# Performance work log

Hardware: AMD Instinct MI355X
Metric: run time of the kernel (lower is better)

## Reference

```python
import jax, jax.numpy as jnp
import numpy as np

B, S, I, E, D = 64, 512, 64, 256, 256  # batch, src_len, input_size, enc_hid, dec_hid


def _lstm_cell(h, c, x, Wih, Whh, b):
    # PyTorch LSTM gate order: i, f, g, o ; b = b_ih + b_hh combined
    z = x @ Wih.T + h @ Whh.T + b
    i, f, g, o = jnp.split(z, 4, axis=-1)
    c = jax.nn.sigmoid(f) * c + jax.nn.sigmoid(i) * jnp.tanh(g)
    h = jax.nn.sigmoid(o) * jnp.tanh(c)
    return h, c


def _run_lstm(x, h0, c0, Wih, Whh, b):
    # x: [B,S,I] -> outputs [B,S,H]
    def step(carry, xt):
        h, c = _lstm_cell(carry[0], carry[1], xt, Wih, Whh, b)
        return (h, c), h
    _, ys = jax.lax.scan(step, (h0, c0), jnp.swapaxes(x, 0, 1))
    return jnp.swapaxes(ys, 0, 1)


def _forward(x, enc_h0, enc_c0, dec_h0, dec_c0, Wih_f, Whh_f, b_f, Wih_b, Whh_b, b_b,
             W_attn, b_attn, v, Wih_d, Whh_d, b_d, W_lin, b_lin):
    b_, s_ = x.shape[0], x.shape[1]
    # bidirectional encoder
    out_f = _run_lstm(x, enc_h0[0], enc_c0[0], Wih_f, Whh_f, b_f)
    out_b = _run_lstm(x[:, ::-1, :], enc_h0[1], enc_c0[1], Wih_b, Whh_b, b_b)[:, ::-1, :]
    enc_out = jnp.concatenate([out_f, out_b], axis=-1)  # [B,S,2E]
    h0d, c0d = dec_h0[0], dec_c0[0]  # decoder re-starts from these EVERY step (faithful)

    @jax.checkpoint
    def dec_step(carry, _):
        y, h_attn = carry  # y: [B,1], h_attn: [B,D]
        dh = h_attn.shape[-1]
        cat = jnp.concatenate(
            [jnp.broadcast_to(h_attn[:, None, :], (b_, s_, dh)), enc_out], axis=-1)
        energy = jnp.tanh(cat @ W_attn.T + b_attn)              # [B,S,D]
        attn = jax.nn.softmax(jnp.einsum('d,bsd->bs', v, energy), axis=1)
        context = jnp.einsum('bs,bse->be', attn, enc_out)       # [B,2E]
        dec_in = jnp.concatenate([y, context], axis=-1)         # [B,1+2E]
        h_new, _c = _lstm_cell(h0d, c0d, dec_in, Wih_d, Whh_d, b_d)
        y_new = jnp.concatenate([h_new, context], axis=-1) @ W_lin.T + b_lin  # [B,1]
        return (y_new, h_new), y_new

    y0 = jnp.zeros((b_, 1), dtype=x.dtype)
    _, ys = jax.lax.scan(dec_step, (y0, h0d), None, length=s_)  # [S,B,1]
    # output_size == 1, so torch's cat-then-[:,1:] equals the stacked per-step ys
    return jnp.swapaxes(ys, 0, 1).reshape(b_, s_)


def setup_inputs() -> dict:
    key = jax.random.key(0)
    ks = jax.random.split(key, 20)
    W = 0.05  # weight scale ~ torch default init magnitude
    rn = lambda k, sh, s: jax.random.normal(k, sh, dtype=jnp.float32) * s
    return {
        'x': rn(ks[0], (B, S, I), 1.0),
        'enc_h0': rn(ks[1], (2, B, E), 1.0),
        'enc_c0': rn(ks[2], (2, B, E), 1.0),
        'dec_h0': rn(ks[3], (1, B, D), 1.0),
        'dec_c0': rn(ks[4], (1, B, D), 1.0),
        'Wih_f': rn(ks[5], (4 * E, I), W),
        'Whh_f': rn(ks[6], (4 * E, E), W),
        'b_f': rn(ks[7], (4 * E,), W),
        'Wih_b': rn(ks[8], (4 * E, I), W),
        'Whh_b': rn(ks[9], (4 * E, E), W),
        'b_b': rn(ks[10], (4 * E,), W),
        'W_attn': rn(ks[11], (D, D + 2 * E), W),
        'b_attn': rn(ks[12], (D,), W),
        'v': jax.random.uniform(ks[13], (D,), dtype=jnp.float32),
        'Wih_d': rn(ks[14], (4 * D, 2 * E + 1), W),
        'Whh_d': rn(ks[15], (4 * D, D), W),
        'b_d': rn(ks[16], (4 * D,), W),
        'W_lin': rn(ks[17], (1, 2 * E + D), W),
        'b_lin': rn(ks[18], (1,), W),
    }


def reference(x, enc_h0, enc_c0, dec_h0, dec_c0, Wih_f, Whh_f, b_f, Wih_b, Whh_b, b_b,
              W_attn, b_attn, v, Wih_d, Whh_d, b_d, W_lin, b_lin):
    return _forward(x, enc_h0, enc_c0, dec_h0, dec_c0, Wih_f, Whh_f, b_f,
                    Wih_b, Whh_b, b_b, W_attn, b_attn, v, Wih_d, Whh_d, b_d,
                    W_lin, b_lin)
```

## Files before the change

### kernel.cpp

```cpp
#include <hip/hip_runtime.h>
#include <hip/hip_bf16.h>

#define NB 64
#define NS 512
#define NI 64
#define NE 256
#define ND 256
#define N4E 1024
#define N4D 1024
#define NTE 512
#define G 4
#define SLICE 128
#define CELLS 64

__device__ __forceinline__ float fsig(float x){
    return __fdividef(1.f, 1.f + __expf(-x));
}
__device__ __forceinline__ float ftanh(float x){
    x = fminf(10.f, fmaxf(-10.f, x));
    float e = __expf(2.f*x);
    return 1.f - __fdividef(2.f, e + 1.f);
}
__device__ __forceinline__ float wave_sum(float v){
    #pragma unroll
    for (int o=32;o>0;o>>=1) v += __shfl_xor(v, o, 64);
    return v;
}
__device__ __forceinline__ float wave_max(float v){
    #pragma unroll
    for (int o=32;o>0;o>>=1) v = fmaxf(v, __shfl_xor(v, o, 64));
    return v;
}
__device__ __forceinline__ float blo(unsigned u){ return __uint_as_float(u<<16); }
__device__ __forceinline__ float bhi(unsigned u){ return __uint_as_float(u & 0xffff0000u); }
__device__ __forceinline__ unsigned short bfbits(float f){
    __hip_bfloat16 h = __float2bfloat16(f);
    return *(unsigned short*)&h;
}
__device__ __forceinline__ float ld_agf(const float* p){
    return __hip_atomic_load(p, __ATOMIC_RELAXED, __HIP_MEMORY_SCOPE_AGENT);
}
__device__ __forceinline__ void st_agf(float* p, float v){
    __hip_atomic_store(p, v, __ATOMIC_RELAXED, __HIP_MEMORY_SCOPE_AGENT);
}

__device__ __forceinline__ void groupbar(unsigned* flags, int b, int q,
                                         unsigned tgt, int tid){
    __syncthreads();
    if (tid == 0)
        __hip_atomic_store(&flags[b*4+q], tgt, __ATOMIC_RELAXED, __HIP_MEMORY_SCOPE_AGENT);
    if (tid < 4){
        while (__hip_atomic_load(&flags[b*4+tid], __ATOMIC_RELAXED,
                                 __HIP_MEMORY_SCOPE_AGENT) < tgt)
            __builtin_amdgcn_s_sleep(1);
    }
    __syncthreads();
}

__global__ void k_transpose(float* __restrict__ dst, const float* __restrict__ src,
                            int R, int C, int ld, int off){
    int idx = blockIdx.x*256 + threadIdx.x;
    if (idx >= R*C) return;
    int r = idx / C, c = idx - r*C;
    dst[(size_t)c*R + r] = src[(size_t)r*ld + off + c];
}
__global__ void k_transpose16(__hip_bfloat16* __restrict__ dst, const float* __restrict__ src,
                              int R, int C, int ld, int off){
    int idx = blockIdx.x*256 + threadIdx.x;
    if (idx >= R*C) return;
    int r = idx / C, c = idx - r*C;
    dst[(size_t)c*R + r] = __float2bfloat16(src[(size_t)r*ld + off + c]);
}

__global__ void k_pack_wy(float* __restrict__ wy, const float* __restrict__ Wih_d){
    int j = blockIdx.x*256 + threadIdx.x;
    if (j < N4D) wy[j] = Wih_d[(size_t)j*(NTE+1)];
}

__global__ void k_pack_wdtg(__hip_bfloat16* __restrict__ dst, const float* __restrict__ Wih_d){
    int idx = blockIdx.x*256 + threadIdx.x;
    int q = idx >> 17, rem = idx & 131071;
    int e = rem >> 8, jj = rem & 255;
    int j = ((jj>>6)<<8) + (q<<6) + (jj&63);
    dst[idx] = __float2bfloat16(Wih_d[(size_t)j*(NTE+1) + 1 + e]);
}

__global__ void k_zc(float* __restrict__ zc, const float* __restrict__ WhhTd,
                     const float* __restrict__ h0d, const float* __restrict__ b_d){
    int b = blockIdx.x, tid = threadIdx.x;
    __shared__ float h0[ND];
    if (tid < ND) h0[tid] = h0d[b*ND + tid];
    __syncthreads();
    for (int j = tid; j < N4D; j += 256){
        float acc = b_d[j];
        #pragma unroll 8
        for (int d=0; d<ND; ++d) acc = fmaf(h0[d], WhhTd[d*N4D + j], acc);
        zc[b*N4D + j] = acc;
    }
}

__global__ void k_dec_init(float* __restrict__ hG, float* __restrict__ yG,
                           unsigned* __restrict__ flags, const float* __restrict__ dec_h0){
    int b = blockIdx.x, tid = threadIdx.x;
    hG[b*ND + tid] = dec_h0[b*ND + tid];
    if (tid < G) yG[b*G + tid] = 0.f;
    if (tid < G) flags[b*G + tid] = 0u;
}

__global__ __launch_bounds__(1024) void k_enc(
    const float* __restrict__ x, const float* __restrict__ eh0, const float* __restrict__ ec0,
    const unsigned* __restrict__ whhTf, const unsigned* __restrict__ wihTf, const float* __restrict__ bf,
    const unsigned* __restrict__ whhTb, const unsigned* __restrict__ wihTb, const float* __restrict__ bb,
    unsigned* __restrict__ eo32)
{
    int bid = blockIdx.x;
    int b = bid & 63, dir = bid >> 6;
    int tid = threadIdx.x;
    int j2 = tid & 511, kh = tid >> 9;
    const unsigned* whh = dir ? whhTb : whhTf;
    const unsigned* wih = dir ? wihTb : wihTf;
    const float* bias = dir ? bb : bf;

    __shared__ __align__(16) float h_l[NE];
    __shared__ __align__(16) float xt[2][NI];
    __shared__ float zp0[N4E], zp1[N4E];

    float2 bias2 = make_float2(0.f, 0.f);
    if (kh == 0) bias2 = ((const float2*)bias)[j2];

    float cst = 0.f;
    if (tid < NE){
        h_l[tid] = eh0[(dir*NB+b)*NE + tid];
        cst      = ec0[(dir*NB+b)*NE + tid];
    }
    {
        int st0 = dir ? (NS-1) : 0;
        if (tid < 16) ((float4*)xt[0])[tid] = ((const float4*)(x + ((size_t)b*NS+st0)*NI))[tid];
    }
    __syncthreads();

    const unsigned* wihK = wih + (size_t)(kh*32)*512 + j2;
    const unsigned* whhK = whh + (size_t)(kh*128)*512 + j2;
    float* zpme = kh ? zp1 : zp0;

    for (int t=0;t<NS;++t){
        int st = dir ? (NS-1-t) : t;
        float4 xpre = make_float4(0.f,0.f,0.f,0.f);
        if (t+1 < NS && tid < 16){
            int stn = dir ? (NS-2-t) : (t+1);
            xpre = ((const float4*)(x + ((size_t)b*NS+stn)*NI))[tid];
        }
        const float* xc = xt[t&1];
        float x0=bias2.x, y0=bias2.y, x1=0.f, y1=0.f;
        #pragma unroll 8
        for (int ii=0; ii<32; ii+=2){
            int i = kh*32 + ii;
            unsigned wa = wihK[(size_t)ii*512];
            unsigned wb = wihK[(size_t)(ii+1)*512];
            float xa = xc[i], xb = xc[i+1];
            x0 = fmaf(xa, blo(wa), x0); y0 = fmaf(xa, bhi(wa), y0);
            x1 = fmaf(xb, blo(wb), x1); y1 = fmaf(xb, bhi(wb), y1);
        }
        #pragma unroll 8
        for (int dd=0; dd<128; dd+=2){
            int d = kh*128 + dd;
            unsigned wa = whhK[(size_t)dd*512];
            unsigned wb = whhK[(size_t)(dd+1)*512];
            float ha = h_l[d], hb = h_l[d+1];
            x0 = fmaf(ha, blo(wa), x0); y0 = fmaf(ha, bhi(wa), y0);
            x1 = fmaf(hb, blo(wb), x1); y1 = fmaf(hb, bhi(wb), y1);
        }
        ((float2*)zpme)[j2] = make_float2(x0+x1, y0+y1);
        if (t+1 < NS && tid < 16) ((float4*)xt[(t+1)&1])[tid] = xpre;
        __syncthreads();
        if (tid < NE){
            int c = tid;
            float zi = zp0[c]        + zp1[c];
            float zf = zp0[NE+c]     + zp1[NE+c];
            float zg = zp0[2*NE+c]   + zp1[2*NE+c];
            float zo = zp0[3*NE+c]   + zp1[3*NE+c];
            cst = fsig(zf)*cst + fsig(zi)*ftanh(zg);
            float hn = fsig(zo)*ftanh(cst);
            h_l[c] = hn;
            ((unsigned short*)eo32)[((size_t)b*NS+st)*NTE + dir*NE + c] = bfbits(hn);
        }
        __syncthreads();
    }
}

__global__ __launch_bounds__(256) void k_encproj(const unsigned* __restrict__ eo32,
        const float* __restrict__ WeT, const float* __restrict__ b_attn,
        unsigned short* __restrict__ ep_pk16){
    int b = blockIdx.y, s0 = blockIdx.x*16, tid = threadIdx.x;
    __shared__ float tile[16*NTE];
    {
        const unsigned* eop = eo32 + (size_t)(b*NS + s0)*256;
        for (int k=0;k<32;++k){
            int wi = k*256 + tid;
            unsigned w = eop[wi];
            int sl = wi>>8, ew = wi&255;
            tile[sl*NTE + 2*ew]   = blo(w);
            tile[sl*NTE + 2*ew+1] = bhi(w);
        }
    }
    __syncthreads();
    float acc[16];
    float ba = b_attn[tid];
    #pragma unroll
    for (int sl=0;sl<16;++sl) acc[sl]=ba;
    #pragma unroll 4
    for (int e4=0;e4<128;++e4){
        float w0 = WeT[(4*e4+0)*ND+tid];
        float w1 = WeT[(4*e4+1)*ND+tid];
        float w2 = WeT[(4*e4+2)*ND+tid];
        float w3 = WeT[(4*e4+3)*ND+tid];
        #pragma unroll
        for (int sl=0;sl<16;++sl){
            const float4 tv = *(const float4*)&tile[sl*NTE + 4*e4];
            acc[sl] = fmaf(tv.x,w0,fmaf(tv.y,w1,fmaf(tv.z,w2,fmaf(tv.w,w3,acc[sl]))));
        }
    }
    #pragma unroll
    for (int sl=0;sl<16;++sl){
        int s = s0+sl;
        size_t wdi = ((size_t)(b*4 + (s>>7))*128 + (tid>>1))*128 + (s&127);
        ep_pk16[wdi*2 + (tid&1)] = bfbits(acc[sl]);
    }
}

__global__ __launch_bounds__(1024, 4) void k_dec(
    const unsigned* __restrict__ eo32,
    const unsigned* __restrict__ ep_pk,
    const unsigned* __restrict__ WhTp,
    const float* __restrict__ v,
    const float* __restrict__ zc, const float* __restrict__ wy,
    const unsigned* __restrict__ WdTp_all,
    const float* __restrict__ dec_c0,
    const float* __restrict__ W_lin, const float* __restrict__ b_lin,
    float* __restrict__ hG, float* __restrict__ yG,
    float* __restrict__ ctxG, float* __restrict__ msG,
    unsigned* __restrict__ flags,
    float* __restrict__ out)
{
    int bid = blockIdx.x;
    int b = bid & 63, q = bid >> 6;
    int tid = threadIdx.x;

    __shared__ unsigned ep_lds[16384];
    __shared__ float part[2048];
    __shared__ float h_l[ND];
    __shared__ float2 hv[ND];
    __shared__ float v_l[ND];
    __shared__ float scores_l[SLICE];
    __shared__ float ctx_l[NTE];
    __shared__ float z_l[256], zc_l[256], wy_l[256];
    __shared__ float c0_l[CELLS], wlh_l[CELLS], wlc_l[SLICE];
    __shared__ float msbuf[8];
    __shared__ float wred[16];
    __shared__ float smax, yprev;

    const unsigned* WdTp = WdTp_all + (size_t)q*NTE*128;

    for (int i=tid; i<16384; i+=1024)
        ep_lds[i] = ep_pk[(size_t)(b*4+q)*16384 + i];
    unsigned eo_reg[32];
    {
        int ep2 = tid & 255, sq = tid >> 8;
        const unsigned* eop = eo32 + (size_t)(b*NS + q*SLICE + sq*32)*256 + ep2;
        #pragma unroll
        for (int ss=0; ss<32; ++ss) eo_reg[ss] = eop[(size_t)ss*256];
    }
    if (tid < 256){
        int jj = tid;
        int j = ((jj>>6)<<8) + (q<<6) + (jj&63);
        zc_l[jj] = zc[b*N4D + j];
        wy_l[jj] = wy[j];
        v_l[tid] = v[tid];
    }
    if (tid < CELLS){
        c0_l[tid]  = dec_c0[b*ND + q*CELLS + tid];
        wlh_l[tid] = W_lin[q*CELLS + tid];
    }
    if (tid < SLICE) wlc_l[tid] = W_lin[ND + q*SLICE + tid];
    float blin = b_lin[0];
    __syncthreads();

    for (int t=0; t<NS; ++t){
        if (tid < ND) h_l[tid] = ld_agf(&hG[b*ND + tid]);
        if (tid == 0){
            float y = 0.f;
            if (t > 0){
                y = blin + ld_agf(&yG[b*G+0]) + ld_agf(&yG[b*G+1])
                         + ld_agf(&yG[b*G+2]) + ld_agf(&yG[b*G+3]);
                if (q == 0) out[(size_t)b*NS + (t-1)] = y;
            }
            yprev = y;
        }
        __syncthreads();
        {
            int d2 = tid & 127, kq = tid >> 7;
            float ax = 0.f, ay = 0.f;
            #pragma unroll 8
            for (int kk=0; kk<32; ++kk){
                int k = kq*32 + kk;
                unsigned w = WhTp[k*128 + d2];
                float hvv = h_l[k];
                ax = fmaf(hvv, blo(w), ax); ay = fmaf(hvv, bhi(w), ay);
            }
            ((float2*)part)[kq*128 + d2] = make_float2(ax, ay);
        }
        __syncthreads();
        if (tid < ND){
            float s = 0.f;
            #pragma unroll
            for (int r=0;r<8;++r) s += part[r*256 + tid];
            hv[tid] = make_float2(v_l[tid], s);
        }
        __syncthreads();
        {
            int sl = tid & 127, dg = tid >> 7;
            float sc = 0.f;
            const unsigned* epl = ep_lds + dg*16*128 + sl;
            #pragma unroll
            for (int k16=0; k16<16; ++k16){
                unsigned w = epl[k16*128];
                int d = dg*32 + 2*k16;
                float2 a0 = hv[d], a1 = hv[d+1];
                sc += a0.x*ftanh(blo(w) + a0.y) + a1.x*ftanh(bhi(w) + a1.y);
            }
            part[dg*128 + sl] = sc;
        }
        __syncthreads();
        if (tid < SLICE){
            float s = 0.f;
            #pragma unroll
            for (int r=0;r<8;++r) s += part[r*128 + tid];
            part[1024 + tid] = s;
            float wm = wave_max(s);
            if ((tid&63)==0) wred[tid>>6] = wm;
        }
        __syncthreads();
        if (tid == 0) smax = fmaxf(wred[0], wred[1]);
        __syncthreads();
        if (tid < SLICE){
            float ev = __expf(part[1024 + tid] - smax);
            scores_l[tid] = ev;
            float s = wave_sum(ev);
            if ((tid&63)==0) wred[2+(tid>>6)] = s;
        }
        __syncthreads();
        if (tid == 0){
            st_agf(&msG[(b*G+q)*2+0], smax);
            st_agf(&msG[(b*G+q)*2+1], wred[2]+wred[3]);
        }
        {
            int ep2 = tid & 255, sq = tid >> 8;
            float ax = 0.f, ay = 0.f;
            #pragma unroll
            for (int ss=0; ss<32; ++ss){
                unsigned w = eo_reg[ss];
                float sc = scores_l[sq*32 + ss];
                ax = fmaf(sc, blo(w), ax); ay = fmaf(sc, bhi(w), ay);
            }
            ((float2*)part)[sq*256 + ep2] = make_float2(ax, ay);
        }
        __syncthreads();
        if (tid < NTE){
            float s = part[tid] + part[512+tid] + part[1024+tid] + part[1536+tid];
            st_agf(&ctxG[(size_t)(b*G+q)*NTE + tid], s);
        }
        groupbar(flags, b, q, (unsigned)(2*t+1), tid);
        float cg0=0.f, cg1=0.f, cg2=0.f, cg3=0.f;
        if (tid < 2*G) msbuf[tid] = ld_agf(&msG[b*G*2 + tid]);
        if (tid < NTE){
            const float* cg = ctxG + (size_t)b*G*NTE + tid;
            cg0 = ld_agf(cg);        cg1 = ld_agf(cg+NTE);
            cg2 = ld_agf(cg+2*NTE);  cg3 = ld_agf(cg+3*NTE);
        }
        __syncthreads();
        float mm = fmaxf(fmaxf(msbuf[0], msbuf[2]), fmaxf(msbuf[4], msbuf[6]));
        float w0 = __expf(msbuf[0]-mm), w1 = __expf(msbuf[2]-mm),
              w2 = __expf(msbuf[4]-mm), w3 = __expf(msbuf[6]-mm);
        float inv = __fdividef(1.f, msbuf[1]*w0 + msbuf[3]*w1 + msbuf[5]*w2 + msbuf[7]*w3);
        if (tid < NTE)
            ctx_l[tid] = (cg0*w0 + cg1*w1 + cg2*w2 + cg3*w3) * inv;
        __syncthreads();
        {
            int jj2 = tid & 127, eq = tid >> 7;
            float ax = 0.f, ay = 0.f;
            #pragma unroll 8
            for (int ee=0; ee<64; ++ee){
                int e = eq*64 + ee;
                unsigned w = WdTp[e*128 + jj2];
                float cv = ctx_l[e];
                ax = fmaf(cv, blo(w), ax); ay = fmaf(cv, bhi(w), ay);
            }
            ((float2*)part)[eq*128 + jj2] = make_float2(ax, ay);
        }
        __syncthreads();
        if (tid < 256){
            float s = zc_l[tid] + yprev*wy_l[tid];
            #pragma unroll
            for (int r=0;r<8;++r) s += part[r*256 + tid];
            z_l[tid] = s;
        }
        __syncthreads();
        float yp = 0.f;
        if (tid < CELLS){
            float zi=z_l[tid], zf=z_l[64+tid], zg=z_l[128+tid], zo=z_l[192+tid];
            float cn = fsig(zf)*c0_l[tid] + fsig(zi)*ftanh(zg);
            float hn = fsig(zo)*ftanh(cn);
            st_agf(&hG[b*ND + q*CELLS + tid], hn);
            yp = hn * wlh_l[tid];
        } else if (tid < CELLS + SLICE){
            yp = ctx_l[q*SLICE + (tid - CELLS)] * wlc_l[tid - CELLS];
        }
        {
            float s = wave_sum(yp);
            if ((tid&63)==0 && tid < 192) wred[8+(tid>>6)] = s;
        }
        __syncthreads();
        if (tid == 0) st_agf(&yG[b*G + q], wred[8]+wred[9]+wred[10]);
        groupbar(flags, b, q, (unsigned)(2*t+2), tid);
    }
    if (q == 0 && tid == 0){
        out[(size_t)b*NS + (NS-1)] = blin + ld_agf(&yG[b*G+0]) + ld_agf(&yG[b*G+1])
                                          + ld_agf(&yG[b*G+2]) + ld_agf(&yG[b*G+3]);
    }
}

extern "C" void kernel_launch(void* const* d_in, const int* in_sizes, int n_in,
                              void* d_out, int out_size, void* d_ws, size_t ws_size,
                              hipStream_t stream){
    const float* x      = (const float*)d_in[0];
    const float* enc_h0 = (const float*)d_in[1];
    const float* enc_c0 = (const float*)d_in[2];
    const float* dec_h0 = (const float*)d_in[3];
    const float* dec_c0 = (const float*)d_in[4];
    const float* Wih_f  = (const float*)d_in[5];
    const float* Whh_f  = (const float*)d_in[6];
    const float* b_f    = (const float*)d_in[7];
    const float* Wih_b  = (const float*)d_in[8];
    const float* Whh_b  = (const float*)d_in[9];
    const float* b_b    = (const float*)d_in[10];
    const float* W_attn = (const float*)d_in[11];
    const float* b_attn = (const float*)d_in[12];
    const float* v      = (const float*)d_in[13];
    const float* Wih_d  = (const float*)d_in[14];
    const float* Whh_d  = (const float*)d_in[15];
    const float* b_d    = (const float*)d_in[16];
    const float* W_lin  = (const float*)d_in[17];
    const float* b_lin  = (const float*)d_in[18];
    float* out = (float*)d_out;
    char* ws   = (char*)d_ws;

    size_t off = 0;
    auto alloc = [&](size_t bytes)->size_t{ size_t o = off; off += (bytes + 255) & ~(size_t)255; return o; };
    size_t o_eo16   = alloc((size_t)NB*NS*NTE*2);
    size_t o_eppk   = alloc((size_t)NB*G*128*128*4);
    size_t o_WihTf  = alloc((size_t)NI*N4E*2);
    size_t o_WhhTf  = alloc((size_t)NE*N4E*2);
    size_t o_WihTb  = alloc((size_t)NI*N4E*2);
    size_t o_WhhTb  = alloc((size_t)NE*N4E*2);
    size_t o_WhT16  = alloc((size_t)ND*ND*2);
    size_t o_WeT    = alloc((size_t)NTE*ND*4);
    size_t o_WdTg   = alloc((size_t)G*NTE*256*2);
    size_t o_WhhTd  = alloc((size_t)ND*N4D*4);
    size_t o_zc     = alloc((size_t)NB*N4D*4);
    size_t o_wy     = alloc((size_t)N4D*4);
    size_t o_hG     = alloc((size_t)NB*ND*4);
    size_t o_yG     = alloc((size_t)NB*G*4);
    size_t o_ctxG   = alloc((size_t)NB*G*NTE*4);
    size_t o_msG    = alloc((size_t)NB*G*2*4);
    size_t o_flags  = alloc((size_t)NB*G*4);
    if (ws_size < off) return;

    auto F   = [&](size_t o)->float*{ return (float*)(ws + o); };
    auto U32 = [&](size_t o)->unsigned*{ return (unsigned*)(ws + o); };
    auto H16 = [&](size_t o)->__hip_bfloat16*{ return (__hip_bfloat16*)(ws + o); };

    auto T32 = [&](size_t dsto, const float* src, int R, int C, int ld, int offc){
        int n = R*C;
        k_transpose<<<dim3((n+255)/256), dim3(256), 0, stream>>>(F(dsto), src, R, C, ld, offc);
    };
    auto T16 = [&](size_t dsto, const float* src, int R, int C, int ld, int offc){
        int n = R*C;
        k_transpose16<<<dim3((n+255)/256), dim3(256), 0, stream>>>(H16(dsto), src, R, C, ld, offc);
    };
    T16(o_WihTf, Wih_f, N4E, NI, NI, 0);
    T16(o_WhhTf, Whh_f, N4E, NE, NE, 0);
    T16(o_WihTb, Wih_b, N4E, NI, NI, 0);
    T16(o_WhhTb, Whh_b, N4E, NE, NE, 0);
    T16(o_WhT16, W_attn, ND, ND, ND+NTE, 0);
    T32(o_WeT,   W_attn, ND, NTE, ND+NTE, ND);
    T32(o_WhhTd, Whh_d, N4D, ND, ND, 0);
    k_pack_wdtg<<<dim3((G*NTE*256)/256), dim3(256), 0, stream>>>(H16(o_WdTg), Wih_d);
    k_pack_wy<<<dim3(4), dim3(256), 0, stream>>>(F(o_wy), Wih_d);
    k_zc<<<dim3(NB), dim3(256), 0, stream>>>(F(o_zc), F(o_WhhTd), dec_h0, b_d);
    k_dec_init<<<dim3(NB), dim3(256), 0, stream>>>(F(o_hG), F(o_yG), (unsigned*)(ws+o_flags), dec_h0);

    k_enc<<<dim3(2*NB), dim3(1024), 0, stream>>>(x, enc_h0, enc_c0,
        U32(o_WhhTf), U32(o_WihTf), b_f, U32(o_WhhTb), U32(o_WihTb), b_b, U32(o_eo16));

    k_encproj<<<dim3(NS/16, NB), dim3(256), 0, stream>>>(U32(o_eo16), F(o_WeT), b_attn,
        (unsigned short*)(ws+o_eppk));

    k_dec<<<dim3(NB*G), dim3(1024), 0, stream>>>(U32(o_eo16), U32(o_eppk),
        U32(o_WhT16), v, F(o_zc), F(o_wy), U32(o_WdTg), dec_c0, W_lin, b_lin,
        F(o_hG), F(o_yG), F(o_ctxG), F(o_msG), (unsigned*)(ws+o_flags), out);
}
```

Baseline: 18.35 ms.

## Split decoder across eight blocks per batch row with wave-local softmax

The decoder now uses 8 cooperating workgroups of 512 threads per batch element instead of 4 of 1024, halving each block's slice of sequence positions and gate rows. Attention scores and the softmax max/sum are now reduced within a wave using shuffles, replacing several block-wide syncs. Context partials are exchanged as 64-bit atomic stores, and the tanh clamp is dropped. The intent is to spread the serial per-step work over more CUs and cut barriers, at the cost of a wider cross-block group barrier (8 flags) and more partial contexts to merge each step.

Result: slower. 32.27 ms (+75.9%).

```diff
diff --git a/kernel.cpp b/kernel.cpp
--- a/kernel.cpp
+++ b/kernel.cpp
@@ -9,26 +9,19 @@
 #define N4E 1024
 #define N4D 1024
 #define NTE 512
-#define G 4
-#define SLICE 128
-#define CELLS 64
+#define G 8
+#define SLICE 64
+#define CELLS 32
 
 __device__ __forceinline__ float fsig(float x){
     return __fdividef(1.f, 1.f + __expf(-x));
 }
 __device__ __forceinline__ float ftanh(float x){
-    x = fminf(10.f, fmaxf(-10.f, x));
-    float e = __expf(2.f*x);
-    return 1.f - __fdividef(2.f, e + 1.f);
+    return 1.f - __fdividef(2.f, 1.f + __expf(2.f*x));
 }
 __device__ __forceinline__ float wave_sum(float v){
     #pragma unroll
     for (int o=32;o>0;o>>=1) v += __shfl_xor(v, o, 64);
-    return v;
-}
-__device__ __forceinline__ float wave_max(float v){
-    #pragma unroll
-    for (int o=32;o>0;o>>=1) v = fmaxf(v, __shfl_xor(v, o, 64));
     return v;
 }
 __device__ __forceinline__ float blo(unsigned u){ return __uint_as_float(u<<16); }
@@ -43,14 +36,20 @@
 __device__ __forceinline__ void st_agf(float* p, float v){
     __hip_atomic_store(p, v, __ATOMIC_RELAXED, __HIP_MEMORY_SCOPE_AGENT);
 }
+__device__ __forceinline__ unsigned long long ld_ag64(const unsigned long long* p){
+    return __hip_atomic_load(p, __ATOMIC_RELAXED, __HIP_MEMORY_SCOPE_AGENT);
+}
+__device__ __forceinline__ void st_ag64(unsigned long long* p, unsigned long long v){
+    __hip_atomic_store(p, v, __ATOMIC_RELAXED, __HIP_MEMORY_SCOPE_AGENT);
+}
 
 __device__ __forceinline__ void groupbar(unsigned* flags, int b, int q,
                                          unsigned tgt, int tid){
     __syncthreads();
     if (tid == 0)
-        __hip_atomic_store(&flags[b*4+q], tgt, __ATOMIC_RELAXED, __HIP_MEMORY_SCOPE_AGENT);
-    if (tid < 4){
-        while (__hip_atomic_load(&flags[b*4+tid], __ATOMIC_RELAXED,
+        __hip_atomic_store(&flags[(b<<5)+q], tgt, __ATOMIC_RELAXED, __HIP_MEMORY_SCOPE_AGENT);
+    if (tid < G){
+        while (__hip_atomic_load(&flags[(b<<5)+tid], __ATOMIC_RELAXED,
                                  __HIP_MEMORY_SCOPE_AGENT) < tgt)
             __builtin_amdgcn_s_sleep(1);
     }
@@ -77,12 +76,12 @@
     if (j < N4D) wy[j] = Wih_d[(size_t)j*(NTE+1)];
 }
 
-__global__ void k_pack_wdtg(__hip_bfloat16* __restrict__ dst, const float* __restrict__ Wih_d){
+__global__ void k_pack_wdtg(unsigned short* __restrict__ dst, const float* __restrict__ Wih_d){
     int idx = blockIdx.x*256 + threadIdx.x;
-    int q = idx >> 17, rem = idx & 131071;
-    int e = rem >> 8, jj = rem & 255;
-    int j = ((jj>>6)<<8) + (q<<6) + (jj&63);
-    dst[idx] = __float2bfloat16(Wih_d[(size_t)j*(NTE+1) + 1 + e]);
+    int q = idx >> 16, rem = idx & 65535;
+    int e = rem >> 7, jj = rem & 127;
+    int j = ((jj>>5)<<8) + (q<<5) + (jj&31);
+    dst[idx] = bfbits(Wih_d[(size_t)j*(NTE+1) + 1 + e]);
 }
 
 __global__ void k_zc(float* __restrict__ zc, const float* __restrict__ WhhTd,
@@ -103,8 +102,7 @@
                            unsigned* __restrict__ flags, const float* __restrict__ dec_h0){
     int b = blockIdx.x, tid = threadIdx.x;
     hG[b*ND + tid] = dec_h0[b*ND + tid];
-    if (tid < G) yG[b*G + tid] = 0.f;
-    if (tid < G) flags[b*G + tid] = 0u;
+    if (tid < G){ yG[(b<<5) + tid] = 0.f; flags[(b<<5) + tid] = 0u; }
 }
 
 __global__ __launch_bounds__(1024) void k_enc(
@@ -223,12 +221,12 @@
     #pragma unroll
     for (int sl=0;sl<16;++sl){
         int s = s0+sl;
-        size_t wdi = ((size_t)(b*4 + (s>>7))*128 + (tid>>1))*128 + (s&127);
+        size_t wdi = (((size_t)(b*8 + (s>>6))*128 + (tid>>1))*64 + (s&63));
         ep_pk16[wdi*2 + (tid&1)] = bfbits(acc[sl]);
     }
 }
 
-__global__ __launch_bounds__(1024, 4) void k_dec(
+__global__ __launch_bounds__(512, 4) void k_dec(
     const unsigned* __restrict__ eo32,
     const unsigned* __restrict__ ep_pk,
     const unsigned* __restrict__ WhTp,
@@ -245,38 +243,42 @@
     int bid = blockIdx.x;
     int b = bid & 63, q = bid >> 6;
     int tid = threadIdx.x;
-
-    __shared__ unsigned ep_lds[16384];
-    __shared__ float part[2048];
-    __shared__ float h_l[ND];
-    __shared__ float2 hv[ND];
-    __shared__ float v_l[ND];
+    int w = tid >> 6, l = tid & 63;
+
+    __shared__ unsigned ep_lds[8192];
+    __shared__ float part[1024];
+    __shared__ float h_l[ND], v_l[ND];
+    __shared__ float2 hvp[8*33];
     __shared__ float scores_l[SLICE];
+    __shared__ float2 msl[8];
+    __shared__ float wsc[8];
     __shared__ float ctx_l[NTE];
-    __shared__ float z_l[256], zc_l[256], wy_l[256];
+    __shared__ float z_l[128], zc_l[128], wy_l[128];
     __shared__ float c0_l[CELLS], wlh_l[CELLS], wlc_l[SLICE];
-    __shared__ float msbuf[8];
-    __shared__ float wred[16];
-    __shared__ float smax, yprev;
-
-    const unsigned* WdTp = WdTp_all + (size_t)q*NTE*128;
-
-    for (int i=tid; i<16384; i+=1024)
-        ep_lds[i] = ep_pk[(size_t)(b*4+q)*16384 + i];
+    __shared__ float msbuf[16];
+    __shared__ float wred[8];
+    __shared__ float yprev_s;
+
+    const unsigned* WdTp = WdTp_all + (size_t)q*NTE*64;
+
+    for (int i=tid; i<8192; i+=512)
+        ep_lds[i] = ep_pk[(size_t)(b*8+q)*8192 + i];
     unsigned eo_reg[32];
     {
-        int ep2 = tid & 255, sq = tid >> 8;
-        const unsigned* eop = eo32 + (size_t)(b*NS + q*SLICE + sq*32)*256 + ep2;
+        int ep2 = w*32 + (l&31), sq = l>>5;
         #pragma unroll
-        for (int ss=0; ss<32; ++ss) eo_reg[ss] = eop[(size_t)ss*256];
-    }
-    if (tid < 256){
+        for (int i=0; i<32; ++i){
+            int s = q*SLICE + sq*32 + ((i + sq*8)&31);
+            eo_reg[i] = eo32[(size_t)(b*NS + s)*256 + ep2];
+        }
+    }
+    if (tid < 128){
         int jj = tid;
-        int j = ((jj>>6)<<8) + (q<<6) + (jj&63);
+        int j = ((jj>>5)<<8) + (q<<5) + (jj&31);
         zc_l[jj] = zc[b*N4D + j];
         wy_l[jj] = wy[j];
-        v_l[tid] = v[tid];
-    }
+    }
+    if (tid < ND) v_l[tid] = v[tid];
     if (tid < CELLS){
         c0_l[tid]  = dec_c0[b*ND + q*CELLS + tid];
         wlh_l[tid] = W_lin[q*CELLS + tid];
@@ -290,142 +292,174 @@
         if (tid == 0){
             float y = 0.f;
             if (t > 0){
-                y = blin + ld_agf(&yG[b*G+0]) + ld_agf(&yG[b*G+1])
-                         + ld_agf(&yG[b*G+2]) + ld_agf(&yG[b*G+3]);
+                y = blin;
+                #pragma unroll
+                for (int qq=0; qq<G; ++qq) y += ld_agf(&yG[(b<<5)+qq]);
                 if (q == 0) out[(size_t)b*NS + (t-1)] = y;
             }
-            yprev = y;
+            yprev_s = y;
         }
         __syncthreads();
         {
             int d2 = tid & 127, kq = tid >> 7;
             float ax = 0.f, ay = 0.f;
             #pragma unroll 8
-            for (int kk=0; kk<32; ++kk){
-                int k = kq*32 + kk;
-                unsigned w = WhTp[k*128 + d2];
+            for (int kk=0; kk<64; ++kk){
+                int k = kq*64 + kk;
+                unsigned ww = WhTp[k*128 + d2];
                 float hvv = h_l[k];
-                ax = fmaf(hvv, blo(w), ax); ay = fmaf(hvv, bhi(w), ay);
+                ax = fmaf(hvv, blo(ww), ax); ay = fmaf(hvv, bhi(ww), ay);
             }
             ((float2*)part)[kq*128 + d2] = make_float2(ax, ay);
         }
         __syncthreads();
         if (tid < ND){
-            float s = 0.f;
-            #pragma unroll
-            for (int r=0;r<8;++r) s += part[r*256 + tid];
-            hv[tid] = make_float2(v_l[tid], s);
+            float s = part[tid] + part[256+tid] + part[512+tid] + part[768+tid];
+            hvp[((tid>>5)*33) + (tid&31)] = make_float2(v_l[tid], s);
         }
         __syncthreads();
         {
-            int sl = tid & 127, dg = tid >> 7;
+            int si = (l>>3)&7, dg = l&7;
+            int s_loc = w*8 + si;
             float sc = 0.f;
-            const unsigned* epl = ep_lds + dg*16*128 + sl;
+            const unsigned* epl = ep_lds + dg*1024 + s_loc;
             #pragma unroll
             for (int k16=0; k16<16; ++k16){
-                unsigned w = epl[k16*128];
-                int d = dg*32 + 2*k16;
-                float2 a0 = hv[d], a1 = hv[d+1];
-                sc += a0.x*ftanh(blo(w) + a0.y) + a1.x*ftanh(bhi(w) + a1.y);
-            }
-            part[dg*128 + sl] = sc;
-        }
-        __syncthreads();
-        if (tid < SLICE){
-            float s = 0.f;
-            #pragma unroll
-            for (int r=0;r<8;++r) s += part[r*128 + tid];
-            part[1024 + tid] = s;
-            float wm = wave_max(s);
-            if ((tid&63)==0) wred[tid>>6] = wm;
-        }
-        __syncthreads();
-        if (tid == 0) smax = fmaxf(wred[0], wred[1]);
-        __syncthreads();
-        if (tid < SLICE){
-            float ev = __expf(part[1024 + tid] - smax);
-            scores_l[tid] = ev;
-            float s = wave_sum(ev);
-            if ((tid&63)==0) wred[2+(tid>>6)] = s;
+                unsigned ww = epl[k16*64];
+                float2 a0 = hvp[dg*33 + 2*k16];
+                float2 a1 = hvp[dg*33 + 2*k16 + 1];
+                sc += a0.x*ftanh(blo(ww) + a0.y) + a1.x*ftanh(bhi(ww) + a1.y);
+            }
+            sc += __shfl_xor(sc, 1, 64);
+            sc += __shfl_xor(sc, 2, 64);
+            sc += __shfl_xor(sc, 4, 64);
+            float m = sc;
+            m = fmaxf(m, __shfl_xor(m, 8, 64));
+            m = fmaxf(m, __shfl_xor(m, 16, 64));
+            m = fmaxf(m, __shfl_xor(m, 32, 64));
+            float ev = __expf(sc - m);
+            float sw = ev;
+            sw += __shfl_xor(sw, 8, 64);
+            sw += __shfl_xor(sw, 16, 64);
+            sw += __shfl_xor(sw, 32, 64);
+            if (dg == 0) scores_l[s_loc] = ev;
+            if (l == 0) msl[w] = make_float2(m, sw);
         }
         __syncthreads();
         if (tid == 0){
-            st_agf(&msG[(b*G+q)*2+0], smax);
-            st_agf(&msG[(b*G+q)*2+1], wred[2]+wred[3]);
-        }
+            float M = msl[0].x;
+            #pragma unroll
+            for (int ww=1; ww<8; ++ww) M = fmaxf(M, msl[ww].x);
+            float S = 0.f;
+            #pragma unroll
+            for (int ww=0; ww<8; ++ww){
+                float sca = __expf(msl[ww].x - M);
+                wsc[ww] = sca;
+                S = fmaf(msl[ww].y, sca, S);
+            }
+            st_agf(&msG[(b<<5) + 2*q + 0], M);
+            st_agf(&msG[(b<<5) + 2*q + 1], S);
+        }
+        __syncthreads();
         {
-            int ep2 = tid & 255, sq = tid >> 8;
+            int ep2 = w*32 + (l&31), sq = l>>5;
             float ax = 0.f, ay = 0.f;
             #pragma unroll
-            for (int ss=0; ss<32; ++ss){
-                unsigned w = eo_reg[ss];
-                float sc = scores_l[sq*32 + ss];
-                ax = fmaf(sc, blo(w), ax); ay = fmaf(sc, bhi(w), ay);
-            }
-            ((float2*)part)[sq*256 + ep2] = make_float2(ax, ay);
-        }
-        __syncthreads();
-        if (tid < NTE){
-            float s = part[tid] + part[512+tid] + part[1024+tid] + part[1536+tid];
-            st_agf(&ctxG[(size_t)(b*G+q)*NTE + tid], s);
+            for (int c=0; c<4; ++c){
+                int si8 = (c + sq) & 3;
+                float wv = wsc[sq*4 + si8];
+                int sbase = sq*32 + si8*8;
+                #pragma unroll
+                for (int ii=0; ii<8; ++ii){
+                    float p = scores_l[sbase + ii] * wv;
+                    unsigned e = eo_reg[c*8 + ii];
+                    ax = fmaf(p, blo(e), ax); ay = fmaf(p, bhi(e), ay);
+                }
+            }
+            ax += __shfl_xor(ax, 32, 64);
+            ay += __shfl_xor(ay, 32, 64);
+            if (l < 32){
+                float2 val = make_float2(ax, ay);
+                st_ag64((unsigned long long*)(ctxG + (size_t)(b*8+q)*NTE + 2*ep2),
+                        *(unsigned long long*)&val);
+            }
         }
         groupbar(flags, b, q, (unsigned)(2*t+1), tid);
-        float cg0=0.f, cg1=0.f, cg2=0.f, cg3=0.f;
-        if (tid < 2*G) msbuf[tid] = ld_agf(&msG[b*G*2 + tid]);
-        if (tid < NTE){
-            const float* cg = ctxG + (size_t)b*G*NTE + tid;
-            cg0 = ld_agf(cg);        cg1 = ld_agf(cg+NTE);
-            cg2 = ld_agf(cg+2*NTE);  cg3 = ld_agf(cg+3*NTE);
-        }
-        __syncthreads();
-        float mm = fmaxf(fmaxf(msbuf[0], msbuf[2]), fmaxf(msbuf[4], msbuf[6]));
-        float w0 = __expf(msbuf[0]-mm), w1 = __expf(msbuf[2]-mm),
-              w2 = __expf(msbuf[4]-mm), w3 = __expf(msbuf[6]-mm);
-        float inv = __fdividef(1.f, msbuf[1]*w0 + msbuf[3]*w1 + msbuf[5]*w2 + msbuf[7]*w3);
-        if (tid < NTE)
-            ctx_l[tid] = (cg0*w0 + cg1*w1 + cg2*w2 + cg3*w3) * inv;
+        unsigned long long cg[8];
+        if (tid < 16) msbuf[tid] = ld_agf(&msG[(b<<5) + tid]);
+        if (tid < 256){
+            const unsigned long long* cgp =
+                (const unsigned long long*)(ctxG + (size_t)b*8*NTE) + tid;
+            #pragma unroll
+            for (int qq=0; qq<8; ++qq) cg[qq] = ld_ag64(cgp + qq*256);
+        }
+        __syncthreads();
+        if (tid < 256){
+            float mm = msbuf[0];
+            #pragma unroll
+            for (int qq=1; qq<8; ++qq) mm = fmaxf(mm, msbuf[2*qq]);
+            float den = 0.f;
+            float wq[8];
+            #pragma unroll
+            for (int qq=0; qq<8; ++qq){
+                wq[qq] = __expf(msbuf[2*qq] - mm);
+                den = fmaf(msbuf[2*qq+1], wq[qq], den);
+            }
+            float inv = __fdividef(1.f, den);
+            float ax = 0.f, ay = 0.f;
+            #pragma unroll
+            for (int qq=0; qq<8; ++qq){
+                float2 c2 = *(float2*)&cg[qq];
+                ax = fmaf(c2.x, wq[qq], ax);
+                ay = fmaf(c2.y, wq[qq], ay);
+            }
+            ((float2*)ctx_l)[tid] = make_float2(ax*inv, ay*inv);
+        }
         __syncthreads();
         {
-            int jj2 = tid & 127, eq = tid >> 7;
+            int jj2 = l, eq = w;
             float ax = 0.f, ay = 0.f;
             #pragma unroll 8
             for (int ee=0; ee<64; ++ee){
                 int e = eq*64 + ee;
-                unsigned w = WdTp[e*128 + jj2];
+                unsigned ww = WdTp[e*64 + jj2];
                 float cv = ctx_l[e];
-                ax = fmaf(cv, blo(w), ax); ay = fmaf(cv, bhi(w), ay);
-            }
-            ((float2*)part)[eq*128 + jj2] = make_float2(ax, ay);
-        }
-        __syncthreads();
-        if (tid < 256){
-            float s = zc_l[tid] + yprev*wy_l[tid];
-            #pragma unroll
-            for (int r=0;r<8;++r) s += part[r*256 + tid];
+                ax = fmaf(cv, blo(ww), ax); ay = fmaf(cv, bhi(ww), ay);
+            }
+            ((float2*)part)[eq*64 + jj2] = make_float2(ax, ay);
+        }
+        __syncthreads();
+        if (tid < 128){
+            float s = zc_l[tid] + yprev_s*wy_l[tid];
+            #pragma unroll
+            for (int r=0; r<8; ++r) s += part[r*128 + tid];
             z_l[tid] = s;
         }
         __syncthreads();
         float yp = 0.f;
         if (tid < CELLS){
-            float zi=z_l[tid], zf=z_l[64+tid], zg=z_l[128+tid], zo=z_l[192+tid];
+            float zi=z_l[tid], zf=z_l[32+tid], zg=z_l[64+tid], zo=z_l[96+tid];
             float cn = fsig(zf)*c0_l[tid] + fsig(zi)*ftanh(zg);
             float hn = fsig(zo)*ftanh(cn);
             st_agf(&hG[b*ND + q*CELLS + tid], hn);
             yp = hn * wlh_l[tid];
-        } else if (tid < CELLS + SLICE){
-            yp = ctx_l[q*SLICE + (tid - CELLS)] * wlc_l[tid - CELLS];
-        }
-        {
+        } else if (tid >= 64 && tid < 64 + SLICE){
+            int i = tid - 64;
+            yp = ctx_l[q*SLICE + i] * wlc_l[i];
+        }
+        if (tid < 128){
             float s = wave_sum(yp);
-            if ((tid&63)==0 && tid < 192) wred[8+(tid>>6)] = s;
-        }
-        __syncthreads();
-        if (tid == 0) st_agf(&yG[b*G + q], wred[8]+wred[9]+wred[10]);
+            if (l == 0) wred[w] = s;
+        }
+        __syncthreads();
+        if (tid == 0) st_agf(&yG[(b<<5) + q], wred[0] + wred[1]);
         groupbar(flags, b, q, (unsigned)(2*t+2), tid);
     }
     if (q == 0 && tid == 0){
-        out[(size_t)b*NS + (NS-1)] = blin + ld_agf(&yG[b*G+0]) + ld_agf(&yG[b*G+1])
-                                          + ld_agf(&yG[b*G+2]) + ld_agf(&yG[b*G+3]);
+        float y = blin;
+        #pragma unroll
+        for (int qq=0; qq<G; ++qq) y += ld_agf(&yG[(b<<5)+qq]);
+        out[(size_t)b*NS + (NS-1)] = y;
     }
 }
 
@@ -457,22 +491,22 @@
     size_t off = 0;
     auto alloc = [&](size_t bytes)->size_t{ size_t o = off; off += (bytes + 255) & ~(size_t)255; return o; };
     size_t o_eo16   = alloc((size_t)NB*NS*NTE*2);
-    size_t o_eppk   = alloc((size_t)NB*G*128*128*4);
+    size_t o_eppk   = alloc((size_t)NB*G*8192*4);
     size_t o_WihTf  = alloc((size_t)NI*N4E*2);
     size_t o_WhhTf  = alloc((size_t)NE*N4E*2);
     size_t o_WihTb  = alloc((size_t)NI*N4E*2);
     size_t o_WhhTb  = alloc((size_t)NE*N4E*2);
     size_t o_WhT16  = alloc((size_t)ND*ND*2);
     size_t o_WeT    = alloc((size_t)NTE*ND*4);
-    size_t o_WdTg   = alloc((size_t)G*NTE*256*2);
+    size_t o_WdTg   = alloc((size_t)G*NTE*128*2);
     size_t o_WhhTd  = alloc((size_t)ND*N4D*4);
     size_t o_zc     = alloc((size_t)NB*N4D*4);
     size_t o_wy     = alloc((size_t)N4D*4);
     size_t o_hG     = alloc((size_t)NB*ND*4);
-    size_t o_yG     = alloc((size_t)NB*G*4);
+    size_t o_yG     = alloc((size_t)NB*32*4);
     size_t o_ctxG   = alloc((size_t)NB*G*NTE*4);
-    size_t o_msG    = alloc((size_t)NB*G*2*4);
-    size_t o_flags  = alloc((size_t)NB*G*4);
+    size_t o_msG    = alloc((size_t)NB*32*4);
+    size_t o_flags  = alloc((size_t)NB*32*4);
     if (ws_size < off) return;
 
     auto F   = [&](size_t o)->float*{ return (float*)(ws + o); };
@@ -494,7 +528,8 @@
     T16(o_WhT16, W_attn, ND, ND, ND+NTE, 0);
     T32(o_WeT,   W_attn, ND, NTE, ND+NTE, ND);
     T32(o_WhhTd, Whh_d, N4D, ND, ND, 0);
-    k_pack_wdtg<<<dim3((G*NTE*256)/256), dim3(256), 0, stream>>>(H16(o_WdTg), Wih_d);
+    k_pack_wdtg<<<dim3((G*NTE*128)/256), dim3(256), 0, stream>>>(
+        (unsigned short*)(ws+o_WdTg), Wih_d);
     k_pack_wy<<<dim3(4), dim3(256), 0, stream>>>(F(o_wy), Wih_d);
     k_zc<<<dim3(NB), dim3(256), 0, stream>>>(F(o_zc), F(o_WhhTd), dec_h0, b_d);
     k_dec_init<<<dim3(NB), dim3(256), 0, stream>>>(F(o_hG), F(o_yG), (unsigned*)(ws+o_flags), dec_h0);
@@ -505,7 +540,7 @@
     k_encproj<<<dim3(NS/16, NB), dim3(256), 0, stream>>>(U32(o_eo16), F(o_WeT), b_attn,
         (unsigned short*)(ws+o_eppk));
 
-    k_dec<<<dim3(NB*G), dim3(1024), 0, stream>>>(U32(o_eo16), U32(o_eppk),
+    k_dec<<<dim3(NB*G), dim3(512), 0, stream>>>(U32(o_eo16), U32(o_eppk),
         U32(o_WhT16), v, F(o_zc), F(o_wy), U32(o_WdTg), dec_c0, W_lin, b_lin,
         F(o_hG), F(o_yG), F(o_ctxG), F(o_msG), (unsigned*)(ws+o_flags), out);
 }
```

## Pad decoder sync flags per batch, shuffle-reduce context, halve matvec threads

Applied to the files above, without the earlier changes.

Pads the per-batch flag, y and softmax-stat arrays to 128-byte strides so different batch groups do not share cache lines while spinning. The context reduction now uses wave shuffles over a remapped register layout instead of a shared-memory pass, and cross-block context exchange uses 64-bit atomic loads and stores. The h and context matvecs run on half the threads with longer loops, which shrinks the partial-sum buffer. The tanh clamp is dropped and the launch-bounds occupancy hint is raised, trading possible register pressure and overflow safety for fewer instructions.

Result: slower. 41.40 ms (+125.6%).

```diff
diff --git a/kernel.cpp b/kernel.cpp
--- a/kernel.cpp
+++ b/kernel.cpp
@@ -17,9 +17,7 @@
     return __fdividef(1.f, 1.f + __expf(-x));
 }
 __device__ __forceinline__ float ftanh(float x){
-    x = fminf(10.f, fmaxf(-10.f, x));
-    float e = __expf(2.f*x);
-    return 1.f - __fdividef(2.f, e + 1.f);
+    return 1.f - __fdividef(2.f, 1.f + __expf(2.f*x));
 }
 __device__ __forceinline__ float wave_sum(float v){
     #pragma unroll
@@ -43,14 +41,20 @@
 __device__ __forceinline__ void st_agf(float* p, float v){
     __hip_atomic_store(p, v, __ATOMIC_RELAXED, __HIP_MEMORY_SCOPE_AGENT);
 }
+__device__ __forceinline__ unsigned long long ld_ag64(const unsigned long long* p){
+    return __hip_atomic_load(p, __ATOMIC_RELAXED, __HIP_MEMORY_SCOPE_AGENT);
+}
+__device__ __forceinline__ void st_ag64(unsigned long long* p, unsigned long long v){
+    __hip_atomic_store(p, v, __ATOMIC_RELAXED, __HIP_MEMORY_SCOPE_AGENT);
+}
 
 __device__ __forceinline__ void groupbar(unsigned* flags, int b, int q,
                                          unsigned tgt, int tid){
     __syncthreads();
     if (tid == 0)
-        __hip_atomic_store(&flags[b*4+q], tgt, __ATOMIC_RELAXED, __HIP_MEMORY_SCOPE_AGENT);
-    if (tid < 4){
-        while (__hip_atomic_load(&flags[b*4+tid], __ATOMIC_RELAXED,
+        __hip_atomic_store(&flags[(b<<5)+q], tgt, __ATOMIC_RELAXED, __HIP_MEMORY_SCOPE_AGENT);
+    if (tid < G){
+        while (__hip_atomic_load(&flags[(b<<5)+tid], __ATOMIC_RELAXED,
                                  __HIP_MEMORY_SCOPE_AGENT) < tgt)
             __builtin_amdgcn_s_sleep(1);
     }
@@ -103,8 +107,7 @@
                            unsigned* __restrict__ flags, const float* __restrict__ dec_h0){
     int b = blockIdx.x, tid = threadIdx.x;
     hG[b*ND + tid] = dec_h0[b*ND + tid];
-    if (tid < G) yG[b*G + tid] = 0.f;
-    if (tid < G) flags[b*G + tid] = 0u;
+    if (tid < G){ yG[(b<<5) + tid] = 0.f; flags[(b<<5) + tid] = 0u; }
 }
 
 __global__ __launch_bounds__(1024) void k_enc(
@@ -228,7 +231,7 @@
     }
 }
 
-__global__ __launch_bounds__(1024, 4) void k_dec(
+__global__ __launch_bounds__(1024, 8) void k_dec(
     const unsigned* __restrict__ eo32,
     const unsigned* __restrict__ ep_pk,
     const unsigned* __restrict__ WhTp,
@@ -245,13 +248,14 @@
     int bid = blockIdx.x;
     int b = bid & 63, q = bid >> 6;
     int tid = threadIdx.x;
+    int w = tid >> 6, l = tid & 63;
 
     __shared__ unsigned ep_lds[16384];
-    __shared__ float part[2048];
+    __shared__ float part[1024];
     __shared__ float h_l[ND];
     __shared__ float2 hv[ND];
-    __shared__ float v_l[ND];
-    __shared__ float scores_l[SLICE];
+    __shared__ float scraw[SLICE];
+    __shared__ float scores_p[4*33];
     __shared__ float ctx_l[NTE];
     __shared__ float z_l[256], zc_l[256], wy_l[256];
     __shared__ float c0_l[CELLS], wlh_l[CELLS], wlc_l[SLICE];
@@ -265,7 +269,7 @@
         ep_lds[i] = ep_pk[(size_t)(b*4+q)*16384 + i];
     unsigned eo_reg[32];
     {
-        int ep2 = tid & 255, sq = tid >> 8;
+        int sq = l & 3, ep2 = w*16 + (l>>2);
         const unsigned* eop = eo32 + (size_t)(b*NS + q*SLICE + sq*32)*256 + ep2;
         #pragma unroll
         for (int ss=0; ss<32; ++ss) eo_reg[ss] = eop[(size_t)ss*256];
@@ -275,8 +279,8 @@
         int j = ((jj>>6)<<8) + (q<<6) + (jj&63);
         zc_l[jj] = zc[b*N4D + j];
         wy_l[jj] = wy[j];
-        v_l[tid] = v[tid];
-    }
+    }
+    if (tid < ND) hv[tid] = make_float2(v[tid], 0.f);
     if (tid < CELLS){
         c0_l[tid]  = dec_c0[b*ND + q*CELLS + tid];
         wlh_l[tid] = W_lin[q*CELLS + tid];
@@ -290,32 +294,28 @@
         if (tid == 0){
             float y = 0.f;
             if (t > 0){
-                y = blin + ld_agf(&yG[b*G+0]) + ld_agf(&yG[b*G+1])
-                         + ld_agf(&yG[b*G+2]) + ld_agf(&yG[b*G+3]);
+                y = blin + ld_agf(&yG[(b<<5)+0]) + ld_agf(&yG[(b<<5)+1])
+                         + ld_agf(&yG[(b<<5)+2]) + ld_agf(&yG[(b<<5)+3]);
                 if (q == 0) out[(size_t)b*NS + (t-1)] = y;
             }
             yprev = y;
         }
         __syncthreads();
-        {
+        if (tid < 512){
             int d2 = tid & 127, kq = tid >> 7;
             float ax = 0.f, ay = 0.f;
             #pragma unroll 8
-            for (int kk=0; kk<32; ++kk){
-                int k = kq*32 + kk;
-                unsigned w = WhTp[k*128 + d2];
+            for (int kk=0; kk<64; ++kk){
+                int k = kq*64 + kk;
+                unsigned ww = WhTp[k*128 + d2];
                 float hvv = h_l[k];
-                ax = fmaf(hvv, blo(w), ax); ay = fmaf(hvv, bhi(w), ay);
+                ax = fmaf(hvv, blo(ww), ax); ay = fmaf(hvv, bhi(ww), ay);
             }
             ((float2*)part)[kq*128 + d2] = make_float2(ax, ay);
         }
         __syncthreads();
-        if (tid < ND){
-            float s = 0.f;
-            #pragma unroll
-            for (int r=0;r<8;++r) s += part[r*256 + tid];
-            hv[tid] = make_float2(v_l[tid], s);
-        }
+        if (tid < ND)
+            hv[tid].y = part[tid] + part[256+tid] + part[512+tid] + part[768+tid];
         __syncthreads();
         {
             int sl = tid & 127, dg = tid >> 7;
@@ -323,10 +323,10 @@
             const unsigned* epl = ep_lds + dg*16*128 + sl;
             #pragma unroll
             for (int k16=0; k16<16; ++k16){
-                unsigned w = epl[k16*128];
+                unsigned ww = epl[k16*128];
                 int d = dg*32 + 2*k16;
                 float2 a0 = hv[d], a1 = hv[d+1];
-                sc += a0.x*ftanh(blo(w) + a0.y) + a1.x*ftanh(bhi(w) + a1.y);
+                sc += a0.x*ftanh(blo(ww) + a0.y) + a1.x*ftanh(bhi(ww) + a1.y);
             }
             part[dg*128 + sl] = sc;
         }
@@ -335,7 +335,7 @@
             float s = 0.f;
             #pragma unroll
             for (int r=0;r<8;++r) s += part[r*128 + tid];
-            part[1024 + tid] = s;
+            scraw[tid] = s;
             float wm = wave_max(s);
             if ((tid&63)==0) wred[tid>>6] = wm;
         }
@@ -343,57 +343,67 @@
         if (tid == 0) smax = fmaxf(wred[0], wred[1]);
         __syncthreads();
         if (tid < SLICE){
-            float ev = __expf(part[1024 + tid] - smax);
-            scores_l[tid] = ev;
+            float ev = __expf(scraw[tid] - smax);
+            scores_p[(tid>>5)*33 + (tid&31)] = ev;
             float s = wave_sum(ev);
             if ((tid&63)==0) wred[2+(tid>>6)] = s;
         }
         __syncthreads();
         if (tid == 0){
-            st_agf(&msG[(b*G+q)*2+0], smax);
-            st_agf(&msG[(b*G+q)*2+1], wred[2]+wred[3]);
+            st_agf(&msG[(b<<5) + 2*q + 0], smax);
+            st_agf(&msG[(b<<5) + 2*q + 1], wred[2]+wred[3]);
         }
         {
-            int ep2 = tid & 255, sq = tid >> 8;
+            int sq = l & 3, ep2 = w*16 + (l>>2);
             float ax = 0.f, ay = 0.f;
+            const float* sp = scores_p + sq*33;
             #pragma unroll
             for (int ss=0; ss<32; ++ss){
-                unsigned w = eo_reg[ss];
-                float sc = scores_l[sq*32 + ss];
-                ax = fmaf(sc, blo(w), ax); ay = fmaf(sc, bhi(w), ay);
+                float p = sp[ss];
+                unsigned e = eo_reg[ss];
+                ax = fmaf(p, blo(e), ax); ay = fmaf(p, bhi(e), ay);
             }
-            ((float2*)part)[sq*256 + ep2] = make_float2(ax, ay);
-        }
-        __syncthreads();
-        if (tid < NTE){
-            float s = part[tid] + part[512+tid] + part[1024+tid] + part[1536+tid];
-            st_agf(&ctxG[(size_t)(b*G+q)*NTE + tid], s);
+            ax += __shfl_xor(ax, 1, 64); ay += __shfl_xor(ay, 1, 64);
+            ax += __shfl_xor(ax, 2, 64); ay += __shfl_xor(ay, 2, 64);
+            if (sq == 0) ((float2*)part)[ep2] = make_float2(ax, ay);
+        }
+        __syncthreads();
+        if (tid < 256){
+            float2 c2 = ((float2*)part)[tid];
+            st_ag64((unsigned long long*)(ctxG + (size_t)(b*4+q)*NTE + 2*tid),
+                    *(unsigned long long*)&c2);
         }
         groupbar(flags, b, q, (unsigned)(2*t+1), tid);
-        float cg0=0.f, cg1=0.f, cg2=0.f, cg3=0.f;
-        if (tid < 2*G) msbuf[tid] = ld_agf(&msG[b*G*2 + tid]);
-        if (tid < NTE){
-            const float* cg = ctxG + (size_t)b*G*NTE + tid;
-            cg0 = ld_agf(cg);        cg1 = ld_agf(cg+NTE);
-            cg2 = ld_agf(cg+2*NTE);  cg3 = ld_agf(cg+3*NTE);
-        }
-        __syncthreads();
-        float mm = fmaxf(fmaxf(msbuf[0], msbuf[2]), fmaxf(msbuf[4], msbuf[6]));
-        float w0 = __expf(msbuf[0]-mm), w1 = __expf(msbuf[2]-mm),
-              w2 = __expf(msbuf[4]-mm), w3 = __expf(msbuf[6]-mm);
-        float inv = __fdividef(1.f, msbuf[1]*w0 + msbuf[3]*w1 + msbuf[5]*w2 + msbuf[7]*w3);
-        if (tid < NTE)
-            ctx_l[tid] = (cg0*w0 + cg1*w1 + cg2*w2 + cg3*w3) * inv;
-        __syncthreads();
-        {
+        unsigned long long cg[4];
+        if (tid < 8) msbuf[tid] = ld_agf(&msG[(b<<5) + tid]);
+        if (tid < 256){
+            const unsigned long long* cgp =
+                (const unsigned long long*)(ctxG + (size_t)b*4*NTE) + tid;
+            #pragma unroll
+            for (int qq=0; qq<4; ++qq) cg[qq] = ld_ag64(cgp + qq*256);
+        }
+        __syncthreads();
+        if (tid < 256){
+            float mm = fmaxf(fmaxf(msbuf[0], msbuf[2]), fmaxf(msbuf[4], msbuf[6]));
+            float w0 = __expf(msbuf[0]-mm), w1 = __expf(msbuf[2]-mm),
+                  w2 = __expf(msbuf[4]-mm), w3 = __expf(msbuf[6]-mm);
+            float inv = __fdividef(1.f, msbuf[1]*w0 + msbuf[3]*w1 + msbuf[5]*w2 + msbuf[7]*w3);
+            float2 c0v = *(float2*)&cg[0], c1v = *(float2*)&cg[1];
+            float2 c2v = *(float2*)&cg[2], c3v = *(float2*)&cg[3];
+            float ax = c0v.x*w0 + c1v.x*w1 + c2v.x*w2 + c3v.x*w3;
+            float ay = c0v.y*w0 + c1v.y*w1 + c2v.y*w2 + c3v.y*w3;
+            ((float2*)ctx_l)[tid] = make_float2(ax*inv, ay*inv);
+        }
+        __syncthreads();
+        if (tid < 512){
             int jj2 = tid & 127, eq = tid >> 7;
             float ax = 0.f, ay = 0.f;
             #pragma unroll 8
-            for (int ee=0; ee<64; ++ee){
-                int e = eq*64 + ee;
-                unsigned w = WdTp[e*128 + jj2];
+            for (int ee=0; ee<128; ++ee){
+                int e = eq*128 + ee;
+                unsigned ww = WdTp[e*128 + jj2];
                 float cv = ctx_l[e];
-                ax = fmaf(cv, blo(w), ax); ay = fmaf(cv, bhi(w), ay);
+                ax = fmaf(cv, blo(ww), ax); ay = fmaf(cv, bhi(ww), ay);
             }
             ((float2*)part)[eq*128 + jj2] = make_float2(ax, ay);
         }
@@ -401,7 +411,7 @@
         if (tid < 256){
             float s = zc_l[tid] + yprev*wy_l[tid];
             #pragma unroll
-            for (int r=0;r<8;++r) s += part[r*256 + tid];
+            for (int r=0; r<4; ++r) s += part[r*256 + tid];
             z_l[tid] = s;
         }
         __syncthreads();
@@ -420,12 +430,12 @@
             if ((tid&63)==0 && tid < 192) wred[8+(tid>>6)] = s;
         }
         __syncthreads();
-        if (tid == 0) st_agf(&yG[b*G + q], wred[8]+wred[9]+wred[10]);
+        if (tid == 0) st_agf(&yG[(b<<5) + q], wred[8]+wred[9]+wred[10]);
         groupbar(flags, b, q, (unsigned)(2*t+2), tid);
     }
     if (q == 0 && tid == 0){
-        out[(size_t)b*NS + (NS-1)] = blin + ld_agf(&yG[b*G+0]) + ld_agf(&yG[b*G+1])
-                                          + ld_agf(&yG[b*G+2]) + ld_agf(&yG[b*G+3]);
+        out[(size_t)b*NS + (NS-1)] = blin + ld_agf(&yG[(b<<5)+0]) + ld_agf(&yG[(b<<5)+1])
+                                          + ld_agf(&yG[(b<<5)+2]) + ld_agf(&yG[(b<<5)+3]);
     }
 }
 
@@ -469,10 +479,10 @@
     size_t o_zc     = alloc((size_t)NB*N4D*4);
     size_t o_wy     = alloc((size_t)N4D*4);
     size_t o_hG     = alloc((size_t)NB*ND*4);
-    size_t o_yG     = alloc((size_t)NB*G*4);
+    size_t o_yG     = alloc((size_t)NB*32*4);
     size_t o_ctxG   = alloc((size_t)NB*G*NTE*4);
-    size_t o_msG    = alloc((size_t)NB*G*2*4);
-    size_t o_flags  = alloc((size_t)NB*G*4);
+    size_t o_msG    = alloc((size_t)NB*32*4);
+    size_t o_flags  = alloc((size_t)NB*32*4);
     if (ws_size < off) return;
 
     auto F   = [&](size_t o)->float*{ return (float*)(ws + o); };
```
